# Optimization experiments

Measured on AMD Instinct MI355X. Metric: run time of the kernel, lower is better.

Reference implementation:

```python
import jax, jax.numpy as jnp
import numpy as np
import math

E = 8          # num_experts
IN = 1024      # input_size
HID = 512      # head_size (expert hidden)
TOP_K = 2
B, P = 8, 1024


def setup_inputs() -> dict:
    key = jax.random.key(0)
    k1, k2, k3, k4, k5 = jax.random.split(key, 5)
    # expert weights init like ParallelExperts.reset_parameters (uniform xavier-ish)
    std1 = math.sqrt(2.0 / (IN + HID)); a1 = math.sqrt(3.0) * std1
    std2 = math.sqrt(2.0 / (HID + IN)); a2 = math.sqrt(3.0) * std2
    return {
        "x": jax.random.normal(k1, (B, P, IN), dtype=jnp.float32),
        "Q_isp": jax.random.normal(k2, (B, P, 1, IN), dtype=jnp.float32),
        "K_isp": jax.random.normal(k3, (B, P, E, IN), dtype=jnp.float32),
        "w1": jax.random.uniform(k4, (E, IN, HID), minval=-a1, maxval=a1, dtype=jnp.float32),
        "w2": jax.random.uniform(k5, (E, HID, IN), minval=-a2, maxval=a2, dtype=jnp.float32),
    }


def _gates(Q_isp, K_isp):
    # attention-based gating, eval path (no noise)
    N = K_isp.shape[2]
    scale = 1.0 / math.sqrt(K_isp.shape[-1])
    # [B,P,1,N] -> [T,N]
    scores = jnp.einsum('bpqd,bpnd->bpqn', Q_isp, K_isp)[:, :, 0, :].reshape(-1, N) * scale
    logits = jnp.nan_to_num(scores, nan=0.0, posinf=20.0, neginf=-20.0)
    probs = jax.nn.softmax(logits, axis=1)
    top_g, top_i = jax.lax.top_k(probs, TOP_K)
    # renormalize top-k gates; denominator detached as in torch (.detach())
    top_g = top_g / jax.lax.stop_gradient(top_g.sum(axis=1, keepdims=True) + 1e-6)
    T = probs.shape[0]
    gates = jnp.zeros_like(probs).at[jnp.arange(T)[:, None], top_i].set(top_g)
    return gates  # [T, E]


def reference(x, Q_isp, K_isp, w1, w2):
    gates = _gates(Q_isp, K_isp)                       # [T,E]
    T = gates.shape[0]
    xt = x.reshape(T, -1)                              # [T,IN]
    # grouped expert GEMMs (dense-masked form; gates are 0 off top-k)
    h = jax.nn.gelu(jnp.einsum('ti,eio->teo', xt, w1), approximate=False)  # [T,E,HID]
    y = jnp.einsum('teo,eoi->tei', h, w2)              # [T,E,IN]
    out = jnp.einsum('tei,te->ti', y, gates)           # combine with gates
    return out.reshape(x.shape)
```

## Files before the change

### kernel.cpp

```cpp
#include <hip/hip_runtime.h>
#include <math.h>

#define TT 8192
#define NE 8
#define DIN 1024
#define DH 512
#define MT_MAX 136

typedef __attribute__((ext_vector_type(8))) short short8;
typedef __attribute__((ext_vector_type(4))) float f32x4;
typedef __attribute__((ext_vector_type(4))) unsigned short us4;

static const size_t NSLOT      = (size_t)(2 * TT + NE * 128);
static const size_t OFF_BASE   = 0;
static const size_t OFF_TOKEXP = 256;
static const size_t OFF_GPAIR  = OFF_TOKEXP + (size_t)TT * 8;
static const size_t OFF_SLOT0  = OFF_GPAIR  + (size_t)TT * 8;
static const size_t OFF_SLOT1  = OFF_SLOT0  + (size_t)TT * 4;
static const size_t OFF_TOK    = OFF_SLOT1  + (size_t)TT * 4;
static const size_t OFF_GATE   = OFF_TOK    + NSLOT * 4;
static const size_t OFF_XB     = OFF_GATE   + NSLOT * 4;
static const size_t OFF_W1T    = OFF_XB     + (size_t)TT * DIN * 2;
static const size_t OFF_W2T    = OFF_W1T    + (size_t)NE * DH * DIN * 2;
static const size_t OFF_H      = OFF_W2T    + (size_t)NE * DIN * DH * 2;
static const size_t OFF_Y      = OFF_H      + NSLOT * DH * 2;

__device__ __forceinline__ unsigned short f2bf(float f) {
    union { float f; unsigned u; } v; v.f = f;
    unsigned r = (v.u + 0x7fffu + ((v.u >> 16) & 1u)) >> 16;
    return (unsigned short)r;
}
__device__ __forceinline__ float bf2f(unsigned short u) {
    union { unsigned u; float f; } v; v.u = ((unsigned)u) << 16;
    return v.f;
}
__device__ __forceinline__ void async_copy16(const void* g, void* l) {
    __builtin_amdgcn_global_load_lds(
        (const __attribute__((address_space(1))) void*)g,
        (__attribute__((address_space(3))) void*)l, 16, 0, 0);
}

__device__ __forceinline__ float gelu_erf(float u) {
    float z  = 0.70710678118f * u;
    float az = fabsf(z);
    float t  = __builtin_amdgcn_rcpf(__builtin_fmaf(0.3275911f, az, 1.0f));
    float p  = t * (0.254829592f + t * (-0.284496736f + t * (1.421413741f +
               t * (-1.453152027f + t * 1.061405429f))));
    float e2 = exp2f(-1.4426950408889634f * az * az);
    float er = __builtin_fmaf(-p, e2, 1.0f);
    er = copysignf(er, z);
    return 0.5f * u * (1.0f + er);
}

__global__ __launch_bounds__(256) void prep_kernel(
    const float* __restrict__ x, const float* __restrict__ w1, const float* __restrict__ w2,
    const float* __restrict__ Q, const float* __restrict__ Kc,
    unsigned short* __restrict__ xb, unsigned short* __restrict__ w1t,
    unsigned short* __restrict__ w2t,
    int2* __restrict__ tokexp, float2* __restrict__ gpair)
{
    __shared__ float tile[32][33];
    int bid = blockIdx.x;
    int tid = threadIdx.x;

    if (bid < 2048) {
        int wave = tid >> 6, lane = tid & 63;
        int t = bid * 4 + wave;
        const float4* q4 = reinterpret_cast<const float4*>(Q + (size_t)t * DIN);
        const float4* k4 = reinterpret_cast<const float4*>(Kc + (size_t)t * NE * DIN);
        float4 q[4];
#pragma unroll
        for (int j = 0; j < 4; ++j) q[j] = q4[j * 64 + lane];
        float part[NE];
#pragma unroll
        for (int e = 0; e < NE; ++e) {
            float s = 0.0f;
#pragma unroll
            for (int j = 0; j < 4; ++j) {
                float4 kv = k4[e * 256 + j * 64 + lane];
                s += q[j].x * kv.x + q[j].y * kv.y + q[j].z * kv.z + q[j].w * kv.w;
            }
            part[e] = s;
        }
#pragma unroll
        for (int e = 0; e < NE; ++e) {
#pragma unroll
            for (int m = 1; m < 64; m <<= 1) part[e] += __shfl_xor(part[e], m);
        }
        if (lane == 0) {
            float s[NE];
#pragma unroll
            for (int e = 0; e < NE; ++e) {
                float v = part[e] * 0.03125f;
                if (isnan(v)) v = 0.0f;
                else if (isinf(v)) v = (v > 0.0f) ? 20.0f : -20.0f;
                s[e] = v;
            }
            float m = s[0];
            for (int e = 1; e < NE; ++e) m = fmaxf(m, s[e]);
            float p[NE]; float sum = 0.0f;
            for (int e = 0; e < NE; ++e) { p[e] = expf(s[e] - m); sum += p[e]; }
            float inv = 1.0f / sum;
            for (int e = 0; e < NE; ++e) p[e] *= inv;
            int i0 = 0;
            for (int e = 1; e < NE; ++e) if (p[e] > p[i0]) i0 = e;
            int i1 = (i0 == 0) ? 1 : 0;
            for (int e = 0; e < NE; ++e) if (e != i0 && p[e] > p[i1]) i1 = e;
            float denom = p[i0] + p[i1] + 1e-6f;
            tokexp[t] = make_int2(i0, i1);
            gpair[t]  = make_float2(p[i0] / denom, p[i1] / denom);
        }
    } else if (bid < 6144) {
        size_t i = ((size_t)(bid - 2048) * 256 + tid) * 8;
        float4 a = *reinterpret_cast<const float4*>(x + i);
        float4 b = *reinterpret_cast<const float4*>(x + i + 4);
        us4 o0 = { f2bf(a.x), f2bf(a.y), f2bf(a.z), f2bf(a.w) };
        us4 o1 = { f2bf(b.x), f2bf(b.y), f2bf(b.z), f2bf(b.w) };
        *reinterpret_cast<us4*>(xb + i)     = o0;
        *reinterpret_cast<us4*>(xb + i + 4) = o1;
    } else {
        const float* src; unsigned short* dst; int K, N, e, k0, n0;
        if (bid < 10240) {
            int r = bid - 6144; e = r >> 9; int rem = r & 511;
            k0 = (rem & 31) * 32; n0 = (rem >> 5) * 32;
            src = w1; dst = w1t; K = DIN; N = DH;
        } else {
            int r = bid - 10240; e = r >> 9; int rem = r & 511;
            k0 = (rem & 15) * 32; n0 = (rem >> 4) * 32;
            src = w2; dst = w2t; K = DH; N = DIN;
        }
        int tx = tid & 31, ty = tid >> 5;
        const float* s = src + ((size_t)e * K + k0) * N + n0;
#pragma unroll
        for (int r2 = 0; r2 < 32; r2 += 8) tile[ty + r2][tx] = s[(size_t)(ty + r2) * N + tx];
        __syncthreads();
        unsigned short* d = dst + ((size_t)e * N + n0) * K + k0;
#pragma unroll
        for (int r2 = 0; r2 < 32; r2 += 8) d[(size_t)(ty + r2) * K + tx] = f2bf(tile[tx][ty + r2]);
    }
}

__global__ __launch_bounds__(1024) void route_kernel(
    const int2* __restrict__ tokexp, const float2* __restrict__ gpair,
    int* __restrict__ base,
    int* __restrict__ tok_list, float* __restrict__ gate_list,
    int* __restrict__ slot0, int* __restrict__ slot1)
{
    int e = blockIdx.x;
    int tid = threadIdx.x;
    int wave = tid >> 6, lane = tid & 63;
    __shared__ int hist[NE];
    __shared__ int wsum[16];
    __shared__ int running;

    if (tid < NE) hist[tid] = 0;
    __syncthreads();

    int lc[NE];
#pragma unroll
    for (int j = 0; j < NE; ++j) lc[j] = 0;
#pragma unroll
    for (int r = 0; r < TT / 1024; ++r) {
        int2 te = tokexp[r * 1024 + tid];
#pragma unroll
        for (int j = 0; j < NE; ++j) lc[j] += (te.x == j ? 1 : 0) + (te.y == j ? 1 : 0);
    }
#pragma unroll
    for (int j = 0; j < NE; ++j) {
        int v = lc[j];
#pragma unroll
        for (int m = 1; m < 64; m <<= 1) v += __shfl_xor(v, m);
        if (lane == 0) atomicAdd(&hist[j], v);
    }
    __syncthreads();

    int basep[NE + 1];
    basep[0] = 0;
#pragma unroll
    for (int j = 0; j < NE; ++j) basep[j + 1] = basep[j] + ((hist[j] + 127) & ~127);

    if (tid == 0) {
        base[e] = basep[e];
        if (e == 0) base[NE] = basep[NE];
        running = basep[e];
    }
    __syncthreads();

    int myb = basep[e];
    int cnt_e = hist[e];
#pragma unroll 1
    for (int r = 0; r < TT / 1024; ++r) {
        int t = r * 1024 + tid;
        int2 te = tokexp[t];
        float2 g = gpair[t];
        bool f0 = (te.x == e), f1 = (te.y == e);
        bool f = f0 || f1;
        unsigned long long mask = __ballot(f);
        int mypos = __popcll(mask & ((1ull << lane) - 1ull));
        if (lane == 0) wsum[wave] = __popcll(mask);
        __syncthreads();
        int off = 0, total = 0;
        for (int w = 0; w < 16; ++w) {
            int c = wsum[w];
            if (w < wave) off += c;
            total += c;
        }
        int pos = running + off + mypos;
        if (f) {
            tok_list[pos]  = t;
            gate_list[pos] = f0 ? g.x : g.y;
            if (f0) slot0[t] = pos; else slot1[t] = pos;
        }
        __syncthreads();
        if (tid == 0) running += total;
        __syncthreads();
    }

    int padn = ((cnt_e + 127) & ~127) - cnt_e;
    if (tid < padn) {
        tok_list[myb + cnt_e + tid]  = 0;
        gate_list[myb + cnt_e + tid] = 0.0f;
    }
}

__global__ __launch_bounds__(256) void gemm1_kernel(
    const unsigned short* __restrict__ xb, const unsigned short* __restrict__ w1t,
    const int* __restrict__ base,
    const int* __restrict__ tok_list, unsigned short* __restrict__ h)
{
    int bv[NE + 1];
#pragma unroll
    for (int i = 0; i <= NE; ++i) bv[i] = base[i];
    int g0 = blockIdx.x * 128;
    if (g0 >= bv[NE]) return;
    int e = 0;
#pragma unroll
    for (int i = 1; i < NE; ++i) if (g0 >= bv[i]) e = i;

    int n0 = blockIdx.y * 128;

    __shared__ __align__(16) char smem[65536];

    int tid = threadIdx.x;
    int w = tid >> 6, lane = tid & 63;
    int wm = w & 1, wn = w >> 1;
    int mcol = lane & 15;
    int kq = (lane >> 4) * 8;

    int ra0 = tok_list[g0 + (2 * w + 0) * 16 + mcol];
    int ra1 = tok_list[g0 + (2 * w + 1) * 16 + mcol];

    const unsigned short* w1e = w1t + (size_t)e * DH * DIN;
    const unsigned short* pa0 = xb + (size_t)ra0 * DIN + kq;
    const unsigned short* pa1 = xb + (size_t)ra1 * DIN + kq;
    const unsigned short* pb0 = w1e + (size_t)(n0 + (2 * w + 0) * 16 + mcol) * DIN + kq;
    const unsigned short* pb1 = w1e + (size_t)(n0 + (2 * w + 1) * 16 + mcol) * DIN + kq;

    int d0 = (2 * w + 0) * 1024;
    int d1 = (2 * w + 1) * 1024;

#define STAGE1(buf, koff) do { \
    async_copy16(pa0 + (koff), (buf) + d0); \
    async_copy16(pa1 + (koff), (buf) + d1); \
    async_copy16(pb0 + (koff), (buf) + 8192 + d0); \
    async_copy16(pb1 + (koff), (buf) + 8192 + d1); \
} while (0)

    f32x4 acc[4][4];
#pragma unroll
    for (int i = 0; i < 4; i++)
#pragma unroll
        for (int j = 0; j < 4; j++) acc[i][j] = {0.f, 0.f, 0.f, 0.f};

    STAGE1(smem + 0 * 16384, 0);
    STAGE1(smem + 1 * 16384, 32);
    STAGE1(smem + 2 * 16384, 64);

    const int NT = DIN / 32;
    for (int t = 0; t < NT; ++t) {
        if (t < NT - 2)       asm volatile("s_waitcnt vmcnt(8)" ::: "memory");
        else if (t == NT - 2) asm volatile("s_waitcnt vmcnt(4)" ::: "memory");
        else                  asm volatile("s_waitcnt vmcnt(0)" ::: "memory");
        __builtin_amdgcn_sched_barrier(0);
        __builtin_amdgcn_s_barrier();
        __builtin_amdgcn_sched_barrier(0);
        if (t + 3 < NT) STAGE1(smem + ((t + 3) & 3) * 16384, (t + 3) * 32);

        const char* cb = smem + (t & 3) * 16384;
        short8 af[4], bfr[4];
#pragma unroll
        for (int mt = 0; mt < 4; ++mt)
            af[mt] = *reinterpret_cast<const short8*>(cb + (wm * 4 + mt) * 1024 + lane * 16);
#pragma unroll
        for (int nt = 0; nt < 4; ++nt)
            bfr[nt] = *reinterpret_cast<const short8*>(cb + 8192 + (wn * 4 + nt) * 1024 + lane * 16);
#pragma unroll
        for (int mt = 0; mt < 4; ++mt)
#pragma unroll
            for (int nt = 0; nt < 4; ++nt)
                acc[mt][nt] = __builtin_amdgcn_mfma_f32_16x16x32_bf16(af[mt], bfr[nt], acc[mt][nt], 0, 0, 0);
        __builtin_amdgcn_sched_barrier(0);
    }
#undef STAGE1

#pragma unroll
    for (int mt = 0; mt < 4; ++mt) {
        int rbase = (wm * 4 + mt) * 16 + ((lane >> 4) * 4);
#pragma unroll
        for (int r = 0; r < 4; ++r) {
            int row = rbase + r;
#pragma unroll
            for (int nt = 0; nt < 4; ++nt) {
                float g = gelu_erf(acc[mt][nt][r]);
                int col = n0 + (wn * 4 + nt) * 16 + mcol;
                h[(size_t)(g0 + row) * DH + col] = f2bf(g);
            }
        }
    }
}

__global__ __launch_bounds__(256) void gemm2_kernel(
    const unsigned short* __restrict__ h, const unsigned short* __restrict__ w2t,
    const int* __restrict__ base,
    const float* __restrict__ gate_list, unsigned short* __restrict__ y)
{
    int bv[NE + 1];
#pragma unroll
    for (int i = 0; i <= NE; ++i) bv[i] = base[i];
    int g0 = blockIdx.x * 128;
    if (g0 >= bv[NE]) return;
    int e = 0;
#pragma unroll
    for (int i = 1; i < NE; ++i) if (g0 >= bv[i]) e = i;

    int n0 = blockIdx.y * 128;

    __shared__ __align__(16) char smem[65536];

    int tid = threadIdx.x;
    int w = tid >> 6, lane = tid & 63;
    int wm = w & 1, wn = w >> 1;
    int mcol = lane & 15;
    int kq = (lane >> 4) * 8;

    const unsigned short* w2e = w2t + (size_t)e * DIN * DH;
    const unsigned short* pa0 = h + (size_t)(g0 + (2 * w + 0) * 16 + mcol) * DH + kq;
    const unsigned short* pa1 = h + (size_t)(g0 + (2 * w + 1) * 16 + mcol) * DH + kq;
    const unsigned short* pb0 = w2e + (size_t)(n0 + (2 * w + 0) * 16 + mcol) * DH + kq;
    const unsigned short* pb1 = w2e + (size_t)(n0 + (2 * w + 1) * 16 + mcol) * DH + kq;

    int d0 = (2 * w + 0) * 1024;
    int d1 = (2 * w + 1) * 1024;

#define STAGE2(buf, koff) do { \
    async_copy16(pa0 + (koff), (buf) + d0); \
    async_copy16(pa1 + (koff), (buf) + d1); \
    async_copy16(pb0 + (koff), (buf) + 8192 + d0); \
    async_copy16(pb1 + (koff), (buf) + 8192 + d1); \
} while (0)

    f32x4 acc[4][4];
#pragma unroll
    for (int i = 0; i < 4; i++)
#pragma unroll
        for (int j = 0; j < 4; j++) acc[i][j] = {0.f, 0.f, 0.f, 0.f};

    STAGE2(smem + 0 * 16384, 0);
    STAGE2(smem + 1 * 16384, 32);
    STAGE2(smem + 2 * 16384, 64);

    const int NT = DH / 32;
    for (int t = 0; t < NT; ++t) {
        if (t < NT - 2)       asm volatile("s_waitcnt vmcnt(8)" ::: "memory");
        else if (t == NT - 2) asm volatile("s_waitcnt vmcnt(4)" ::: "memory");
        else                  asm volatile("s_waitcnt vmcnt(0)" ::: "memory");
        __builtin_amdgcn_sched_barrier(0);
        __builtin_amdgcn_s_barrier();
        __builtin_amdgcn_sched_barrier(0);
        if (t + 3 < NT) STAGE2(smem + ((t + 3) & 3) * 16384, (t + 3) * 32);

        const char* cb = smem + (t & 3) * 16384;
        short8 af[4], bfr[4];
#pragma unroll
        for (int mt = 0; mt < 4; ++mt)
            af[mt] = *reinterpret_cast<const short8*>(cb + (wm * 4 + mt) * 1024 + lane * 16);
#pragma unroll
        for (int nt = 0; nt < 4; ++nt)
            bfr[nt] = *reinterpret_cast<const short8*>(cb + 8192 + (wn * 4 + nt) * 1024 + lane * 16);
#pragma unroll
        for (int mt = 0; mt < 4; ++mt)
#pragma unroll
            for (int nt = 0; nt < 4; ++nt)
                acc[mt][nt] = __builtin_amdgcn_mfma_f32_16x16x32_bf16(af[mt], bfr[nt], acc[mt][nt], 0, 0, 0);
        __builtin_amdgcn_sched_barrier(0);
    }
#undef STAGE2

#pragma unroll
    for (int mt = 0; mt < 4; ++mt) {
        int rbase = (wm * 4 + mt) * 16 + ((lane >> 4) * 4);
#pragma unroll
        for (int r = 0; r < 4; ++r) {
            int row = rbase + r;
            float g = gate_list[g0 + row];
#pragma unroll
            for (int nt = 0; nt < 4; ++nt) {
                int col = n0 + (wn * 4 + nt) * 16 + mcol;
                y[(size_t)(g0 + row) * DIN + col] = f2bf(acc[mt][nt][r] * g);
            }
        }
    }
}

__global__ __launch_bounds__(256) void combine_kernel(
    const unsigned short* __restrict__ y,
    const int* __restrict__ slot0, const int* __restrict__ slot1,
    float* __restrict__ out)
{
    int c = threadIdx.x * 4;
#pragma unroll
    for (int r = 0; r < 4; ++r) {
        int t = blockIdx.x * 4 + r;
        const unsigned short* y0 = y + (size_t)slot0[t] * DIN + c;
        const unsigned short* y1 = y + (size_t)slot1[t] * DIN + c;
        us4 u0 = *reinterpret_cast<const us4*>(y0);
        us4 u1 = *reinterpret_cast<const us4*>(y1);
        float4 o;
        o.x = bf2f(u0.x) + bf2f(u1.x);
        o.y = bf2f(u0.y) + bf2f(u1.y);
        o.z = bf2f(u0.z) + bf2f(u1.z);
        o.w = bf2f(u0.w) + bf2f(u1.w);
        *reinterpret_cast<float4*>(out + (size_t)t * DIN + c) = o;
    }
}

extern "C" void kernel_launch(void* const* d_in, const int* in_sizes, int n_in,
                              void* d_out, int out_size, void* d_ws, size_t ws_size,
                              hipStream_t stream) {
    const float* x  = (const float*)d_in[0];
    const float* Q  = (const float*)d_in[1];
    const float* K  = (const float*)d_in[2];
    const float* w1 = (const float*)d_in[3];
    const float* w2 = (const float*)d_in[4];
    float* out = (float*)d_out;

    char* ws = (char*)d_ws;
    int*    base      = (int*)(ws + OFF_BASE);
    int2*   tokexp    = (int2*)(ws + OFF_TOKEXP);
    float2* gpair     = (float2*)(ws + OFF_GPAIR);
    int*    slot0     = (int*)(ws + OFF_SLOT0);
    int*    slot1     = (int*)(ws + OFF_SLOT1);
    int*    tok_list  = (int*)(ws + OFF_TOK);
    float*  gate_list = (float*)(ws + OFF_GATE);
    unsigned short* xb  = (unsigned short*)(ws + OFF_XB);
    unsigned short* w1t = (unsigned short*)(ws + OFF_W1T);
    unsigned short* w2t = (unsigned short*)(ws + OFF_W2T);
    unsigned short* h   = (unsigned short*)(ws + OFF_H);
    unsigned short* y   = (unsigned short*)(ws + OFF_Y);

    prep_kernel<<<14336, 256, 0, stream>>>(x, w1, w2, Q, K, xb, w1t, w2t, tokexp, gpair);
    route_kernel<<<NE, 1024, 0, stream>>>(tokexp, gpair, base, tok_list, gate_list, slot0, slot1);
    gemm1_kernel<<<dim3(MT_MAX, DH / 128), 256, 0, stream>>>(xb, w1t, base, tok_list, h);
    gemm2_kernel<<<dim3(MT_MAX, DIN / 128), 256, 0, stream>>>(h, w2t, base, gate_list, y);
    combine_kernel<<<TT / 4, 256, 0, stream>>>(y, slot0, slot1, out);
}
```

Baseline: 541.1 us.

## Use 64x64 weight transpose tiles, 3-stage GEMM pipeline, and wider combine loads

Result: no change. 544.3 us (+0.6%).

```diff
diff --git a/kernel.cpp b/kernel.cpp
--- a/kernel.cpp
+++ b/kernel.cpp
@@ -10,6 +10,7 @@
 typedef __attribute__((ext_vector_type(8))) short short8;
 typedef __attribute__((ext_vector_type(4))) float f32x4;
 typedef __attribute__((ext_vector_type(4))) unsigned short us4;
+typedef __attribute__((ext_vector_type(2))) unsigned short us2;
 
 static const size_t NSLOT      = (size_t)(2 * TT + NE * 128);
 static const size_t OFF_BASE   = 0;
@@ -59,7 +60,7 @@
     unsigned short* __restrict__ w2t,
     int2* __restrict__ tokexp, float2* __restrict__ gpair)
 {
-    __shared__ float tile[32][33];
+    __shared__ float tile[64][65];
     int bid = blockIdx.x;
     int tid = threadIdx.x;
 
@@ -120,23 +121,27 @@
         *reinterpret_cast<us4*>(xb + i + 4) = o1;
     } else {
         const float* src; unsigned short* dst; int K, N, e, k0, n0;
-        if (bid < 10240) {
-            int r = bid - 6144; e = r >> 9; int rem = r & 511;
-            k0 = (rem & 31) * 32; n0 = (rem >> 5) * 32;
+        if (bid < 7168) {
+            int r = bid - 6144; e = r >> 7; int rem = r & 127;
+            k0 = (rem & 15) * 64; n0 = (rem >> 4) * 64;
             src = w1; dst = w1t; K = DIN; N = DH;
         } else {
-            int r = bid - 10240; e = r >> 9; int rem = r & 511;
-            k0 = (rem & 15) * 32; n0 = (rem >> 4) * 32;
+            int r = bid - 7168; e = r >> 7; int rem = r & 127;
+            k0 = (rem & 7) * 64; n0 = (rem >> 3) * 64;
             src = w2; dst = w2t; K = DH; N = DIN;
         }
-        int tx = tid & 31, ty = tid >> 5;
+        int tx = tid & 63, ty = tid >> 6;
         const float* s = src + ((size_t)e * K + k0) * N + n0;
 #pragma unroll
-        for (int r2 = 0; r2 < 32; r2 += 8) tile[ty + r2][tx] = s[(size_t)(ty + r2) * N + tx];
+        for (int r2 = 0; r2 < 64; r2 += 4) tile[ty + r2][tx] = s[(size_t)(ty + r2) * N + tx];
         __syncthreads();
+        int kx = (tid & 31) * 2, ny = tid >> 5;
         unsigned short* d = dst + ((size_t)e * N + n0) * K + k0;
 #pragma unroll
-        for (int r2 = 0; r2 < 32; r2 += 8) d[(size_t)(ty + r2) * K + tx] = f2bf(tile[tx][ty + r2]);
+        for (int r2 = 0; r2 < 64; r2 += 8) {
+            us2 v = { f2bf(tile[kx][ny + r2]), f2bf(tile[kx + 1][ny + r2]) };
+            *reinterpret_cast<us2*>(d + (size_t)(ny + r2) * K + kx) = v;
+        }
     }
 }
 
@@ -239,7 +244,7 @@
 
     int n0 = blockIdx.y * 128;
 
-    __shared__ __align__(16) char smem[65536];
+    __shared__ __align__(16) char smem[49152];
 
     int tid = threadIdx.x;
     int w = tid >> 6, lane = tid & 63;
@@ -274,19 +279,18 @@
 
     STAGE1(smem + 0 * 16384, 0);
     STAGE1(smem + 1 * 16384, 32);
-    STAGE1(smem + 2 * 16384, 64);
 
     const int NT = DIN / 32;
+    int sc = 0, sn = 2;
     for (int t = 0; t < NT; ++t) {
-        if (t < NT - 2)       asm volatile("s_waitcnt vmcnt(8)" ::: "memory");
-        else if (t == NT - 2) asm volatile("s_waitcnt vmcnt(4)" ::: "memory");
-        else                  asm volatile("s_waitcnt vmcnt(0)" ::: "memory");
+        if (t < NT - 1) asm volatile("s_waitcnt vmcnt(4)" ::: "memory");
+        else            asm volatile("s_waitcnt vmcnt(0)" ::: "memory");
         __builtin_amdgcn_sched_barrier(0);
         __builtin_amdgcn_s_barrier();
         __builtin_amdgcn_sched_barrier(0);
-        if (t + 3 < NT) STAGE1(smem + ((t + 3) & 3) * 16384, (t + 3) * 32);
-
-        const char* cb = smem + (t & 3) * 16384;
+        if (t + 2 < NT) STAGE1(smem + sn * 16384, (t + 2) * 32);
+
+        const char* cb = smem + sc * 16384;
         short8 af[4], bfr[4];
 #pragma unroll
         for (int mt = 0; mt < 4; ++mt)
@@ -300,6 +304,8 @@
             for (int nt = 0; nt < 4; ++nt)
                 acc[mt][nt] = __builtin_amdgcn_mfma_f32_16x16x32_bf16(af[mt], bfr[nt], acc[mt][nt], 0, 0, 0);
         __builtin_amdgcn_sched_barrier(0);
+        sc = (sc == 2) ? 0 : sc + 1;
+        sn = (sn == 2) ? 0 : sn + 1;
     }
 #undef STAGE1
 
@@ -335,7 +341,7 @@
 
     int n0 = blockIdx.y * 128;
 
-    __shared__ __align__(16) char smem[65536];
+    __shared__ __align__(16) char smem[49152];
 
     int tid = threadIdx.x;
     int w = tid >> 6, lane = tid & 63;
@@ -367,19 +373,18 @@
 
     STAGE2(smem + 0 * 16384, 0);
     STAGE2(smem + 1 * 16384, 32);
-    STAGE2(smem + 2 * 16384, 64);
 
     const int NT = DH / 32;
+    int sc = 0, sn = 2;
     for (int t = 0; t < NT; ++t) {
-        if (t < NT - 2)       asm volatile("s_waitcnt vmcnt(8)" ::: "memory");
-        else if (t == NT - 2) asm volatile("s_waitcnt vmcnt(4)" ::: "memory");
-        else                  asm volatile("s_waitcnt vmcnt(0)" ::: "memory");
+        if (t < NT - 1) asm volatile("s_waitcnt vmcnt(4)" ::: "memory");
+        else            asm volatile("s_waitcnt vmcnt(0)" ::: "memory");
         __builtin_amdgcn_sched_barrier(0);
         __builtin_amdgcn_s_barrier();
         __builtin_amdgcn_sched_barrier(0);
-        if (t + 3 < NT) STAGE2(smem + ((t + 3) & 3) * 16384, (t + 3) * 32);
-
-        const char* cb = smem + (t & 3) * 16384;
+        if (t + 2 < NT) STAGE2(smem + sn * 16384, (t + 2) * 32);
+
+        const char* cb = smem + sc * 16384;
         short8 af[4], bfr[4];
 #pragma unroll
         for (int mt = 0; mt < 4; ++mt)
@@ -393,6 +398,8 @@
             for (int nt = 0; nt < 4; ++nt)
                 acc[mt][nt] = __builtin_amdgcn_mfma_f32_16x16x32_bf16(af[mt], bfr[nt], acc[mt][nt], 0, 0, 0);
         __builtin_amdgcn_sched_barrier(0);
+        sc = (sc == 2) ? 0 : sc + 1;
+        sn = (sn == 2) ? 0 : sn + 1;
     }
 #undef STAGE2
 
@@ -417,20 +424,24 @@
     const int* __restrict__ slot0, const int* __restrict__ slot1,
     float* __restrict__ out)
 {
-    int c = threadIdx.x * 4;
+    int tpair = threadIdx.x >> 7;
+    int c = (threadIdx.x & 127) * 8;
 #pragma unroll
     for (int r = 0; r < 4; ++r) {
-        int t = blockIdx.x * 4 + r;
-        const unsigned short* y0 = y + (size_t)slot0[t] * DIN + c;
-        const unsigned short* y1 = y + (size_t)slot1[t] * DIN + c;
-        us4 u0 = *reinterpret_cast<const us4*>(y0);
-        us4 u1 = *reinterpret_cast<const us4*>(y1);
-        float4 o;
-        o.x = bf2f(u0.x) + bf2f(u1.x);
-        o.y = bf2f(u0.y) + bf2f(u1.y);
-        o.z = bf2f(u0.z) + bf2f(u1.z);
-        o.w = bf2f(u0.w) + bf2f(u1.w);
-        *reinterpret_cast<float4*>(out + (size_t)t * DIN + c) = o;
+        int t = blockIdx.x * 8 + r * 2 + tpair;
+        short8 u0 = *reinterpret_cast<const short8*>(y + (size_t)slot0[t] * DIN + c);
+        short8 u1 = *reinterpret_cast<const short8*>(y + (size_t)slot1[t] * DIN + c);
+        float4 o0, o1;
+        o0.x = bf2f((unsigned short)u0[0]) + bf2f((unsigned short)u1[0]);
+        o0.y = bf2f((unsigned short)u0[1]) + bf2f((unsigned short)u1[1]);
+        o0.z = bf2f((unsigned short)u0[2]) + bf2f((unsigned short)u1[2]);
+        o0.w = bf2f((unsigned short)u0[3]) + bf2f((unsigned short)u1[3]);
+        o1.x = bf2f((unsigned short)u0[4]) + bf2f((unsigned short)u1[4]);
+        o1.y = bf2f((unsigned short)u0[5]) + bf2f((unsigned short)u1[5]);
+        o1.z = bf2f((unsigned short)u0[6]) + bf2f((unsigned short)u1[6]);
+        o1.w = bf2f((unsigned short)u0[7]) + bf2f((unsigned short)u1[7]);
+        *reinterpret_cast<float4*>(out + (size_t)t * DIN + c)     = o0;
+        *reinterpret_cast<float4*>(out + (size_t)t * DIN + c + 4) = o1;
     }
 }
 
@@ -458,9 +469,9 @@
     unsigned short* h   = (unsigned short*)(ws + OFF_H);
     unsigned short* y   = (unsigned short*)(ws + OFF_Y);
 
-    prep_kernel<<<14336, 256, 0, stream>>>(x, w1, w2, Q, K, xb, w1t, w2t, tokexp, gpair);
+    prep_kernel<<<8192, 256, 0, stream>>>(x, w1, w2, Q, K, xb, w1t, w2t, tokexp, gpair);
     route_kernel<<<NE, 1024, 0, stream>>>(tokexp, gpair, base, tok_list, gate_list, slot0, slot1);
     gemm1_kernel<<<dim3(MT_MAX, DH / 128), 256, 0, stream>>>(xb, w1t, base, tok_list, h);
     gemm2_kernel<<<dim3(MT_MAX, DIN / 128), 256, 0, stream>>>(h, w2t, base, gate_list, y);
-    combine_kernel<<<TT / 4, 256, 0, stream>>>(y, slot0, slot1, out);
-}
+    combine_kernel<<<TT / 8, 256, 0, stream>>>(y, slot0, slot1, out);
+}
```
